# Kernel tuning notes

Hardware: AMD Instinct MI355X
Metric: run time of the kernel (lower is better)

The kernel has to match this reference:

```python
import jax, jax.numpy as jnp
import numpy as np

B, N, DIM = 4, 2048, 512
HEADS, DK = 8, 64
SCALE = DK ** -0.5


def setup_inputs() -> dict:
    key = jax.random.key(0)
    k1, k2, k3, k4 = jax.random.split(key, 4)
    x = jax.random.normal(k1, (B, N, DIM), dtype=jnp.float32)
    # nn.Linear(dim, dim_key*heads, bias=False): y = x @ W.T; store W already transposed
    Wq = jax.random.normal(k2, (DIM, HEADS * DK), dtype=jnp.float32) * (DIM ** -0.5)
    Wk = jax.random.normal(k3, (DIM, HEADS * DK), dtype=jnp.float32) * (DIM ** -0.5)
    rel_content_bias = jax.random.normal(k4, (1, HEADS, 1, DK), dtype=jnp.float32)
    return {"x": x, "Wq": Wq, "Wk": Wk, "rel_content_bias": rel_content_bias}


def _split_heads(t, h):
    # [b, n, h*d] -> [b, h, n, d]
    b, n, hd = t.shape
    return t.reshape(b, n, h, hd // h).transpose(0, 2, 1, 3)


def reference(x, Wq, Wk, rel_content_bias):
    q = _split_heads(x @ Wq, HEADS) * SCALE          # [b, h, n, dk]
    k = _split_heads(x @ Wk, HEADS)                  # [b, h, n, dk]
    v = _split_heads(x, HEADS)                       # [b, h, n, dim/h]
    logits = jnp.einsum('bhid,bhjd->bhij', q + rel_content_bias, k)
    attn = jax.nn.sigmoid(logits)                    # no softmax normalization
    out = jnp.einsum('bhij,bhjd->bhid', attn, v)     # [b, h, n, dim/h]
    b, h, n, d = out.shape
    return out.transpose(0, 2, 1, 3).reshape(b, n, h * d)
```

## Files before the change

kernel.cpp:

```cpp
#include <hip/hip_runtime.h>
#include <hip/hip_bf16.h>
#include <stdint.h>

#define BB 4
#define NN 2048
#define DIMD 512
#define HH 8
#define DKK 64
#define MTOT (BB * NN)
constexpr float SCALE = 0.125f;

typedef __attribute__((ext_vector_type(4))) float f32x4;
typedef __attribute__((ext_vector_type(8))) short bf16x8;
typedef __attribute__((ext_vector_type(4))) _Float16 f16x4;
typedef __attribute__((ext_vector_type(2))) __fp16 fp16v2;
typedef __attribute__((ext_vector_type(4))) __fp16 fp16v4;

union pack8 { unsigned short s[8]; uint4 v; };

__device__ __forceinline__ unsigned short f2bf(float f) {
  union { float f; uint32_t u; } v; v.f = f;
  uint32_t u = v.u;
  return (unsigned short)((u + 0x7FFFu + ((u >> 16) & 1u)) >> 16);
}

__device__ __forceinline__ unsigned short f2h(float f) {
  union { _Float16 h; unsigned short u; } c; c.h = (_Float16)f;
  return c.u;
}

__device__ __forceinline__ float sigmoidf(float x) {
  return __builtin_amdgcn_rcpf(1.0f + __expf(-x));
}

__global__ __launch_bounds__(256) void prep_x(const float* __restrict__ x,
                                              unsigned short* __restrict__ xb,
                                              unsigned short* __restrict__ xtf) {
  __shared__ __align__(16) unsigned short T[64][72];
  const int b = blockIdx.z, nt = blockIdx.x, dt = blockIdx.y;
  const int tid = threadIdx.x;
  const int n0 = nt * 64, d0 = dt * 64;
  const float* src = x + ((size_t)b * NN + n0) * DIMD + d0;
#pragma unroll
  for (int r = 0; r < 2; r++) {
    int idx = tid + r * 256;
    int nl = idx >> 3, c = idx & 7;
    const float* sp = src + (size_t)nl * DIMD + c * 8;
    pack8 pb;
#pragma unroll
    for (int k = 0; k < 8; k++) {
      float f = sp[k];
      pb.s[k] = f2bf(f);
      T[c * 8 + k][nl] = f2h(f);
    }
    *(uint4*)(xb + ((size_t)b * NN + n0 + nl) * DIMD + d0 + c * 8) = pb.v;
  }
  __syncthreads();
  unsigned short* dst = xtf + ((size_t)b * DIMD + d0) * NN + n0;
#pragma unroll
  for (int r = 0; r < 2; r++) {
    int idx = tid + r * 256;
    int dl = idx >> 3, c = idx & 7;
    uint4 v = *(const uint4*)&T[dl][c * 8];
    *(uint4*)(dst + (size_t)dl * NN + c * 8) = v;
  }
}

__global__ __launch_bounds__(256) void prep_w(const float* __restrict__ wq,
                                              const float* __restrict__ wk,
                                              unsigned short* __restrict__ wtq,
                                              unsigned short* __restrict__ wtk) {
  __shared__ __align__(16) unsigned short T[64][72];
  const float* w = blockIdx.z ? wk : wq;
  unsigned short* wt = blockIdx.z ? wtk : wtq;
  const int kt = blockIdx.x, nt = blockIdx.y;
  const int tid = threadIdx.x;
  const int k0 = kt * 64, n0 = nt * 64;
#pragma unroll
  for (int r = 0; r < 16; r++) {
    int idx = tid + r * 256;
    int kl = idx >> 6, nl = idx & 63;
    T[nl][kl] = f2bf(w[(size_t)(k0 + kl) * DIMD + n0 + nl]);
  }
  __syncthreads();
#pragma unroll
  for (int r = 0; r < 2; r++) {
    int idx = tid + r * 256;
    int nl = idx >> 3, c = idx & 7;
    uint4 v = *(const uint4*)&T[nl][c * 8];
    *(uint4*)(wt + (size_t)(n0 + nl) * DIMD + k0 + c * 8) = v;
  }
}

__global__ __launch_bounds__(256) void qk_gemm(const unsigned short* __restrict__ xb,
                                               const unsigned short* __restrict__ wtq,
                                               const unsigned short* __restrict__ wtk,
                                               const float* __restrict__ bias,
                                               unsigned short* __restrict__ qout,
                                               unsigned short* __restrict__ kout) {
  __shared__ __align__(16) unsigned short Als[128][72];
  __shared__ __align__(16) unsigned short Bls[128][72];
  const int mb = blockIdx.x, nb = blockIdx.y;
  const bool isQ = (nb < 4);
  const unsigned short* wt = isQ ? wtq : wtk;
  unsigned short* outp = isQ ? qout : kout;
  const int n0 = (nb & 3) * 128, m0 = mb * 128;
  const int tid = threadIdx.x;
  const int wave = tid >> 6, lane = tid & 63;
  const int quad = lane >> 4, l16 = lane & 15;
  const int wm = wave >> 1, wn = wave & 1;

  f32x4 acc[4][4];
#pragma unroll
  for (int a = 0; a < 4; a++)
#pragma unroll
    for (int c = 0; c < 4; c++) acc[a][c] = (f32x4){0.f, 0.f, 0.f, 0.f};

  for (int k0 = 0; k0 < DIMD; k0 += 64) {
    __syncthreads();
#pragma unroll
    for (int r = 0; r < 4; r++) {
      int idx = tid + r * 256;
      int row = idx >> 3, c = idx & 7;
      *(uint4*)&Als[row][c * 8] =
          *(const uint4*)(xb + (size_t)(m0 + row) * DIMD + k0 + c * 8);
      *(uint4*)&Bls[row][c * 8] =
          *(const uint4*)(wt + (size_t)(n0 + row) * DIMD + k0 + c * 8);
    }
    __syncthreads();
#pragma unroll
    for (int ks = 0; ks < 2; ks++) {
      bf16x8 af[4], bfr[4];
#pragma unroll
      for (int t = 0; t < 4; t++) {
        af[t] = *(const bf16x8*)&Als[wm * 64 + t * 16 + l16][quad * 8 + ks * 32];
        bfr[t] = *(const bf16x8*)&Bls[wn * 64 + t * 16 + l16][quad * 8 + ks * 32];
      }
#pragma unroll
      for (int tm = 0; tm < 4; tm++)
#pragma unroll
        for (int tn = 0; tn < 4; tn++)
          acc[tm][tn] =
              __builtin_amdgcn_mfma_f32_16x16x32_bf16(af[tm], bfr[tn], acc[tm][tn], 0, 0, 0);
    }
  }
#pragma unroll
  for (int tm = 0; tm < 4; tm++) {
#pragma unroll
    for (int tn = 0; tn < 4; tn++) {
#pragma unroll
      for (int r = 0; r < 4; r++) {
        int row = m0 + wm * 64 + tm * 16 + quad * 4 + r;
        int gcol = n0 + wn * 64 + tn * 16 + l16;
        float v = acc[tm][tn][r];
        if (isQ) v = v * SCALE + bias[gcol];
        outp[(size_t)row * DIMD + gcol] = f2bf(v);
      }
    }
  }
}

__global__ __launch_bounds__(256) void attn(const unsigned short* __restrict__ qb,
                                            const unsigned short* __restrict__ kb,
                                            const unsigned short* __restrict__ xtf,
                                            float* __restrict__ out) {
  __shared__ __align__(16) unsigned short Kls[128][72];
  __shared__ __align__(16) unsigned short Vtls[64][136];
  const int it = blockIdx.x, bh = blockIdx.y;
  const int b = bh >> 3, h = bh & 7;
  const int i0 = it * 64;
  const int tid = threadIdx.x;
  const int wave = tid >> 6, lane = tid & 63;
  const int quad = lane >> 4, l16 = lane & 15;

  const int irow = i0 + wave * 16 + l16;
  bf16x8 qfrag0, qfrag1;
  {
    const unsigned short* qp = qb + ((size_t)b * NN + irow) * DIMD + h * DKK + quad * 8;
    qfrag0 = *(const bf16x8*)qp;
    qfrag1 = *(const bf16x8*)(qp + 32);
  }

  f32x4 o[4];
#pragma unroll
  for (int td = 0; td < 4; td++) o[td] = (f32x4){0.f, 0.f, 0.f, 0.f};

  const unsigned short* kbase = kb + (size_t)b * NN * DIMD + h * DKK;
  const unsigned short* vbase = xtf + ((size_t)b * DIMD + h * DKK) * NN;

  for (int j0 = 0; j0 < NN; j0 += 128) {
    __syncthreads();
#pragma unroll
    for (int r = 0; r < 4; r++) {
      int idx = tid + r * 256;
      int row = idx >> 3, c = idx & 7;
      *(uint4*)&Kls[row][c * 8] =
          *(const uint4*)(kbase + (size_t)(j0 + row) * DIMD + c * 8);
      int rowd = idx >> 4, cv = idx & 15;
      *(uint4*)&Vtls[rowd][cv * 8] =
          *(const uint4*)(vbase + (size_t)rowd * NN + j0 + cv * 8);
    }
    __syncthreads();

#pragma unroll
    for (int t = 0; t < 8; t++) {
      bf16x8 kf0 = *(const bf16x8*)&Kls[t * 16 + l16][quad * 8];
      bf16x8 kf1 = *(const bf16x8*)&Kls[t * 16 + l16][quad * 8 + 32];
      f32x4 sv = (f32x4){0.f, 0.f, 0.f, 0.f};
      sv = __builtin_amdgcn_mfma_f32_16x16x32_bf16(kf0, qfrag0, sv, 0, 0, 0);
      sv = __builtin_amdgcn_mfma_f32_16x16x32_bf16(kf1, qfrag1, sv, 0, 0, 0);
      fp16v2 lo = __builtin_amdgcn_cvt_pkrtz(sigmoidf(sv[0]), sigmoidf(sv[1]));
      fp16v2 hi = __builtin_amdgcn_cvt_pkrtz(sigmoidf(sv[2]), sigmoidf(sv[3]));
      fp16v4 p;
      p.x = lo.x; p.y = lo.y; p.z = hi.x; p.w = hi.y;
      f16x4 pfrag = __builtin_bit_cast(f16x4, p);
#pragma unroll
      for (int td = 0; td < 4; td++) {
        f16x4 vf = *(const f16x4*)&Vtls[td * 16 + l16][t * 16 + quad * 4];
        o[td] = __builtin_amdgcn_mfma_f32_16x16x16f16(vf, pfrag, o[td], 0, 0, 0);
      }
    }
  }

#pragma unroll
  for (int td = 0; td < 4; td++) {
    float* op = out + ((size_t)b * NN + irow) * DIMD + h * DKK + td * 16 + quad * 4;
    *(f32x4*)op = o[td];
  }
}

extern "C" void kernel_launch(void* const* d_in, const int* in_sizes, int n_in,
                              void* d_out, int out_size, void* d_ws, size_t ws_size,
                              hipStream_t stream) {
  const float* x = (const float*)d_in[0];
  const float* Wq = (const float*)d_in[1];
  const float* Wk = (const float*)d_in[2];
  const float* bias = (const float*)d_in[3];
  float* out = (float*)d_out;

  unsigned short* ws = (unsigned short*)d_ws;
  unsigned short* xb = ws;
  unsigned short* xtf = xb + (size_t)MTOT * DIMD;
  unsigned short* wtq = xtf + (size_t)MTOT * DIMD;
  unsigned short* wtk = wtq + (size_t)DIMD * DIMD;
  unsigned short* qb = wtk + (size_t)DIMD * DIMD;
  unsigned short* kb = qb + (size_t)MTOT * DIMD;

  prep_x<<<dim3(32, 8, 4), 256, 0, stream>>>(x, xb, xtf);
  prep_w<<<dim3(8, 8, 2), 256, 0, stream>>>(Wq, Wk, wtq, wtk);
  qk_gemm<<<dim3(64, 8), 256, 0, stream>>>(xb, wtq, wtk, bias, qb, kb);
  attn<<<dim3(32, 32), 256, 0, stream>>>(qb, kb, xtf, out);
}
```

Baseline: 174.8 us.

## Split attention over key halves with 512-thread blocks, polynomial sigmoid, padded LDS

The attention kernel now gives each block 128 query rows and 512 threads. Two 256-thread groups each handle half of the key range and their partial outputs are reduced through LDS. Each wave handles two 16-row query subtiles, so every K and V fragment is reused twice. The sigmoid is replaced by an exp(-|x|) cubic polynomial approximation with sign restoration, which avoids the reciprocal but adds approximation error. LDS row pitch changes to 68 with 8-byte split loads and stores, to reduce bank conflicts in both the GEMM and attention kernels.

```diff
diff --git a/kernel.cpp b/kernel.cpp
--- a/kernel.cpp
+++ b/kernel.cpp
@@ -11,12 +11,15 @@
 constexpr float SCALE = 0.125f;
 
 typedef __attribute__((ext_vector_type(4))) float f32x4;
+typedef __attribute__((ext_vector_type(2))) float f32x2;
 typedef __attribute__((ext_vector_type(8))) short bf16x8;
 typedef __attribute__((ext_vector_type(4))) _Float16 f16x4;
 typedef __attribute__((ext_vector_type(2))) __fp16 fp16v2;
 typedef __attribute__((ext_vector_type(4))) __fp16 fp16v4;
+typedef __attribute__((ext_vector_type(2))) unsigned int u32x2;
 
 union pack8 { unsigned short s[8]; uint4 v; };
+union fragu { u32x2 h[2]; bf16x8 v; };
 
 __device__ __forceinline__ unsigned short f2bf(float f) {
   union { float f; uint32_t u; } v; v.f = f;
@@ -29,8 +32,42 @@
   return c.u;
 }
 
-__device__ __forceinline__ float sigmoidf(float x) {
-  return __builtin_amdgcn_rcpf(1.0f + __expf(-x));
+__device__ __forceinline__ bf16x8 ld_frag(const unsigned short* p) {
+  fragu f;
+  f.h[0] = *(const u32x2*)p;
+  f.h[1] = *(const u32x2*)(p + 4);
+  return f.v;
+}
+__device__ __forceinline__ void st8(unsigned short* p, uint4 v) {
+  *(u32x2*)p = (u32x2){v.x, v.y};
+  *(u32x2*)(p + 4) = (u32x2){v.z, v.w};
+}
+
+__device__ __forceinline__ f16x4 sig_pack(f32x4 sv) {
+  float e0 = __expf(-__builtin_fabsf(sv[0]));
+  float e1 = __expf(-__builtin_fabsf(sv[1]));
+  float e2 = __expf(-__builtin_fabsf(sv[2]));
+  float e3 = __expf(-__builtin_fabsf(sv[3]));
+  const f32x2 c3 = {-0.22184f, -0.22184f};
+  const f32x2 c2 = {0.66550f, 0.66550f};
+  const f32x2 c1 = {-0.94280f, -0.94280f};
+  const f32x2 c0 = {0.49826f, 0.49826f};
+  f32x2 eA = {e0, e1}, eB = {e2, e3};
+  f32x2 pA = __builtin_elementwise_fma(
+      __builtin_elementwise_fma(__builtin_elementwise_fma(c3, eA, c2), eA, c1),
+      eA, c0);
+  f32x2 pB = __builtin_elementwise_fma(
+      __builtin_elementwise_fma(__builtin_elementwise_fma(c3, eB, c2), eB, c1),
+      eB, c0);
+  float r0 = __builtin_copysignf(pA.x, sv[0]) + 0.5f;
+  float r1 = __builtin_copysignf(pA.y, sv[1]) + 0.5f;
+  float r2 = __builtin_copysignf(pB.x, sv[2]) + 0.5f;
+  float r3 = __builtin_copysignf(pB.y, sv[3]) + 0.5f;
+  fp16v2 lo = __builtin_amdgcn_cvt_pkrtz(r0, r1);
+  fp16v2 hi = __builtin_amdgcn_cvt_pkrtz(r2, r3);
+  fp16v4 p;
+  p.x = lo.x; p.y = lo.y; p.z = hi.x; p.w = hi.y;
+  return __builtin_bit_cast(f16x4, p);
 }
 
 __global__ __launch_bounds__(256) void prep_x(const float* __restrict__ x,
@@ -98,8 +135,8 @@
                                                const float* __restrict__ bias,
                                                unsigned short* __restrict__ qout,
                                                unsigned short* __restrict__ kout) {
-  __shared__ __align__(16) unsigned short Als[128][72];
-  __shared__ __align__(16) unsigned short Bls[128][72];
+  __shared__ __align__(16) unsigned short Als[128][68];
+  __shared__ __align__(16) unsigned short Bls[128][68];
   const int mb = blockIdx.x, nb = blockIdx.y;
   const bool isQ = (nb < 4);
   const unsigned short* wt = isQ ? wtq : wtk;
@@ -122,10 +159,8 @@
     for (int r = 0; r < 4; r++) {
       int idx = tid + r * 256;
       int row = idx >> 3, c = idx & 7;
-      *(uint4*)&Als[row][c * 8] =
-          *(const uint4*)(xb + (size_t)(m0 + row) * DIMD + k0 + c * 8);
-      *(uint4*)&Bls[row][c * 8] =
-          *(const uint4*)(wt + (size_t)(n0 + row) * DIMD + k0 + c * 8);
+      st8(&Als[row][c * 8], *(const uint4*)(xb + (size_t)(m0 + row) * DIMD + k0 + c * 8));
+      st8(&Bls[row][c * 8], *(const uint4*)(wt + (size_t)(n0 + row) * DIMD + k0 + c * 8));
     }
     __syncthreads();
 #pragma unroll
@@ -133,8 +168,8 @@
       bf16x8 af[4], bfr[4];
 #pragma unroll
       for (int t = 0; t < 4; t++) {
-        af[t] = *(const bf16x8*)&Als[wm * 64 + t * 16 + l16][quad * 8 + ks * 32];
-        bfr[t] = *(const bf16x8*)&Bls[wn * 64 + t * 16 + l16][quad * 8 + ks * 32];
+        af[t] = ld_frag(&Als[wm * 64 + t * 16 + l16][quad * 8 + ks * 32]);
+        bfr[t] = ld_frag(&Bls[wn * 64 + t * 16 + l16][quad * 8 + ks * 32]);
       }
 #pragma unroll
       for (int tm = 0; tm < 4; tm++)
@@ -160,72 +195,100 @@
   }
 }
 
-__global__ __launch_bounds__(256) void attn(const unsigned short* __restrict__ qb,
-                                            const unsigned short* __restrict__ kb,
-                                            const unsigned short* __restrict__ xtf,
-                                            float* __restrict__ out) {
-  __shared__ __align__(16) unsigned short Kls[128][72];
-  __shared__ __align__(16) unsigned short Vtls[64][136];
+__global__ __launch_bounds__(512, 4) void attn(const unsigned short* __restrict__ qb,
+                                               const unsigned short* __restrict__ kb,
+                                               const unsigned short* __restrict__ xtf,
+                                               float* __restrict__ out) {
+  __shared__ __align__(16) char smem[34816];
+  unsigned short* Kbase = (unsigned short*)smem;
+  unsigned short* Vbase = Kbase + 2 * 64 * 68;
+  float* Obuf = (float*)smem;
+
   const int it = blockIdx.x, bh = blockIdx.y;
   const int b = bh >> 3, h = bh & 7;
-  const int i0 = it * 64;
+  const int i0 = it * 128;
   const int tid = threadIdx.x;
-  const int wave = tid >> 6, lane = tid & 63;
+  const int lane = tid & 63;
+  const int grp = tid >> 8;
+  const int wv = (tid >> 6) & 3;
+  const int gtid = tid & 255;
   const int quad = lane >> 4, l16 = lane & 15;
 
-  const int irow = i0 + wave * 16 + l16;
-  bf16x8 qfrag0, qfrag1;
-  {
-    const unsigned short* qp = qb + ((size_t)b * NN + irow) * DIMD + h * DKK + quad * 8;
-    qfrag0 = *(const bf16x8*)qp;
-    qfrag1 = *(const bf16x8*)(qp + 32);
-  }
-
-  f32x4 o[4];
-#pragma unroll
-  for (int td = 0; td < 4; td++) o[td] = (f32x4){0.f, 0.f, 0.f, 0.f};
+  bf16x8 qf[2][2];
+  int irow[2];
+#pragma unroll
+  for (int s_ = 0; s_ < 2; s_++) {
+    irow[s_] = i0 + wv * 32 + s_ * 16 + l16;
+    const unsigned short* qp = qb + ((size_t)b * NN + irow[s_]) * DIMD + h * DKK + quad * 8;
+    qf[s_][0] = *(const bf16x8*)qp;
+    qf[s_][1] = *(const bf16x8*)(qp + 32);
+  }
+
+  f32x4 o[2][4];
+#pragma unroll
+  for (int s_ = 0; s_ < 2; s_++)
+#pragma unroll
+    for (int td = 0; td < 4; td++) o[s_][td] = (f32x4){0.f, 0.f, 0.f, 0.f};
 
   const unsigned short* kbase = kb + (size_t)b * NN * DIMD + h * DKK;
   const unsigned short* vbase = xtf + ((size_t)b * DIMD + h * DKK) * NN;
-
-  for (int j0 = 0; j0 < NN; j0 += 128) {
+  unsigned short* Kg = Kbase + grp * (64 * 68);
+  unsigned short* Vg = Vbase + grp * (64 * 68);
+  const int jbase = grp * 1024;
+
+  for (int itr = 0; itr < 16; itr++) {
+    const int j0 = jbase + itr * 64;
     __syncthreads();
 #pragma unroll
-    for (int r = 0; r < 4; r++) {
-      int idx = tid + r * 256;
+    for (int r = 0; r < 2; r++) {
+      int idx = gtid + r * 256;
       int row = idx >> 3, c = idx & 7;
-      *(uint4*)&Kls[row][c * 8] =
-          *(const uint4*)(kbase + (size_t)(j0 + row) * DIMD + c * 8);
-      int rowd = idx >> 4, cv = idx & 15;
-      *(uint4*)&Vtls[rowd][cv * 8] =
-          *(const uint4*)(vbase + (size_t)rowd * NN + j0 + cv * 8);
+      st8(&Kg[row * 68 + c * 8], *(const uint4*)(kbase + (size_t)(j0 + row) * DIMD + c * 8));
+      st8(&Vg[row * 68 + c * 8], *(const uint4*)(vbase + (size_t)row * NN + j0 + c * 8));
     }
     __syncthreads();
 
 #pragma unroll
-    for (int t = 0; t < 8; t++) {
-      bf16x8 kf0 = *(const bf16x8*)&Kls[t * 16 + l16][quad * 8];
-      bf16x8 kf1 = *(const bf16x8*)&Kls[t * 16 + l16][quad * 8 + 32];
-      f32x4 sv = (f32x4){0.f, 0.f, 0.f, 0.f};
-      sv = __builtin_amdgcn_mfma_f32_16x16x32_bf16(kf0, qfrag0, sv, 0, 0, 0);
-      sv = __builtin_amdgcn_mfma_f32_16x16x32_bf16(kf1, qfrag1, sv, 0, 0, 0);
-      fp16v2 lo = __builtin_amdgcn_cvt_pkrtz(sigmoidf(sv[0]), sigmoidf(sv[1]));
-      fp16v2 hi = __builtin_amdgcn_cvt_pkrtz(sigmoidf(sv[2]), sigmoidf(sv[3]));
-      fp16v4 p;
-      p.x = lo.x; p.y = lo.y; p.z = hi.x; p.w = hi.y;
-      f16x4 pfrag = __builtin_bit_cast(f16x4, p);
+    for (int t = 0; t < 4; t++) {
+      bf16x8 kf0 = ld_frag(&Kg[(t * 16 + l16) * 68 + quad * 8]);
+      bf16x8 kf1 = ld_frag(&Kg[(t * 16 + l16) * 68 + quad * 8 + 32]);
+      f16x4 pf[2];
+#pragma unroll
+      for (int s_ = 0; s_ < 2; s_++) {
+        f32x4 sv = (f32x4){0.f, 0.f, 0.f, 0.f};
+        sv = __builtin_amdgcn_mfma_f32_16x16x32_bf16(kf0, qf[s_][0], sv, 0, 0, 0);
+        sv = __builtin_amdgcn_mfma_f32_16x16x32_bf16(kf1, qf[s_][1], sv, 0, 0, 0);
+        pf[s_] = sig_pack(sv);
+      }
 #pragma unroll
       for (int td = 0; td < 4; td++) {
-        f16x4 vf = *(const f16x4*)&Vtls[td * 16 + l16][t * 16 + quad * 4];
-        o[td] = __builtin_amdgcn_mfma_f32_16x16x16f16(vf, pfrag, o[td], 0, 0, 0);
-      }
-    }
-  }
-
-#pragma unroll
-  for (int td = 0; td < 4; td++) {
-    float* op = out + ((size_t)b * NN + irow) * DIMD + h * DKK + td * 16 + quad * 4;
-    *(f32x4*)op = o[td];
+        f16x4 vf = __builtin_bit_cast(
+            f16x4, *(const u32x2*)&Vg[(td * 16 + l16) * 68 + t * 16 + quad * 4]);
+        o[0][td] = __builtin_amdgcn_mfma_f32_16x16x16f16(vf, pf[0], o[0][td], 0, 0, 0);
+        o[1][td] = __builtin_amdgcn_mfma_f32_16x16x16f16(vf, pf[1], o[1][td], 0, 0, 0);
+      }
+    }
+  }
+
+  __syncthreads();
+  if (grp == 1) {
+#pragma unroll
+    for (int s_ = 0; s_ < 2; s_++)
+#pragma unroll
+      for (int td = 0; td < 4; td++)
+        *(f32x4*)&Obuf[(wv * 32 + s_ * 16 + l16) * 68 + td * 16 + quad * 4] = o[s_][td];
+  }
+  __syncthreads();
+  if (grp == 0) {
+#pragma unroll
+    for (int s_ = 0; s_ < 2; s_++) {
+#pragma unroll
+      for (int td = 0; td < 4; td++) {
+        o[s_][td] += *(const f32x4*)&Obuf[(wv * 32 + s_ * 16 + l16) * 68 + td * 16 + quad * 4];
+        float* op = out + ((size_t)b * NN + irow[s_]) * DIMD + h * DKK + td * 16 + quad * 4;
+        *(f32x4*)op = o[s_][td];
+      }
+    }
   }
 }
 
@@ -249,5 +312,5 @@
   prep_x<<<dim3(32, 8, 4), 256, 0, stream>>>(x, xb, xtf);
   prep_w<<<dim3(8, 8, 2), 256, 0, stream>>>(Wq, Wk, wtq, wtk);
   qk_gemm<<<dim3(64, 8), 256, 0, stream>>>(xb, wtq, wtk, bias, qb, kb);
-  attn<<<dim3(32, 32), 256, 0, stream>>>(qb, kb, xtf, out);
-}
+  attn<<<dim3(16, 32), 512, 0, stream>>>(qb, kb, xtf, out);
+}
```

After: 159.5 us. 1.1x faster.
